# Kernel optimization log

Hardware: AMD Instinct MI355X
Metric: run time of the kernel (lower is better)

Reference implementation:

```python
import jax, jax.numpy as jnp
import numpy as np
import math

EMBED_DIM = 1024
NUM_HEADS = 16
B, T = 4, 2048
HEAD_DIM = EMBED_DIM // NUM_HEADS


def setup_inputs() -> dict:
    key = jax.random.key(0)
    ks = jax.random.split(key, 9)
    s = 1.0 / math.sqrt(EMBED_DIM)
    x = jax.random.normal(ks[0], (B, T, EMBED_DIM), dtype=jnp.float32)
    # causal mask, broadcastable over (B, H)
    mask = jnp.tril(jnp.ones((T, T), dtype=bool))[None, None, :, :]
    Wq = jax.random.normal(ks[1], (EMBED_DIM, EMBED_DIM), dtype=jnp.float32) * s
    bq = jnp.zeros((EMBED_DIM,), dtype=jnp.float32)
    Wk = jax.random.normal(ks[2], (EMBED_DIM, EMBED_DIM), dtype=jnp.float32) * s
    bk = jnp.zeros((EMBED_DIM,), dtype=jnp.float32)
    Wv = jax.random.normal(ks[3], (EMBED_DIM, EMBED_DIM), dtype=jnp.float32) * s
    bv = jnp.zeros((EMBED_DIM,), dtype=jnp.float32)
    Wo = jax.random.normal(ks[4], (EMBED_DIM, EMBED_DIM), dtype=jnp.float32) * s
    bo = jnp.zeros((EMBED_DIM,), dtype=jnp.float32)
    return {"x": x, "mask": mask, "Wq": Wq, "bq": bq, "Wk": Wk, "bk": bk,
            "Wv": Wv, "bv": bv, "Wo": Wo, "bo": bo}


def reference(x, mask, Wq, bq, Wk, bk, Wv, bv, Wo, bo):
    Bsz, Tlen, C = x.shape
    H, D = NUM_HEADS, HEAD_DIM
    q = (x @ Wq + bq).reshape(Bsz, Tlen, H, D).transpose(0, 2, 1, 3)  # [B,H,T,D]
    k = (x @ Wk + bk).reshape(Bsz, Tlen, H, D).transpose(0, 2, 1, 3)
    v = (x @ Wv + bv).reshape(Bsz, Tlen, H, D).transpose(0, 2, 1, 3)
    scores = jnp.einsum('bhtd,bhsd->bhts', q, k) / math.sqrt(D)  # [B,H,T,T]
    scores = jnp.where(mask, scores, jnp.float32(-1e9))
    attn = jax.nn.softmax(scores, axis=-1)
    out = jnp.einsum('bhts,bhsd->bhtd', attn, v)  # [B,H,T,D]
    out = out.transpose(0, 2, 1, 3).reshape(Bsz, Tlen, C)
    return out @ Wo + bo
```

## Files before the change

kernel.cpp:

```cpp
#include <hip/hip_runtime.h>

#define SEQ   2048
#define NH    16
#define HD    64
#define EMB   1024
#define NB    4
#define MTOT  (NB*SEQ)
#define NT    (SEQ/64)

typedef _Float16 f16;
typedef _Float16 f16x4 __attribute__((ext_vector_type(4)));
typedef _Float16 f16x8 __attribute__((ext_vector_type(8)));
typedef float    f32x4 __attribute__((ext_vector_type(4)));

#define MFMA_F16(a,b,c) __builtin_amdgcn_mfma_f32_16x16x32_f16(a,b,c,0,0,0)

#define QSCALE 0.18033688011112043f

__device__ __forceinline__ float fast_exp2(float x) {
#if __has_builtin(__builtin_amdgcn_exp2f)
  return __builtin_amdgcn_exp2f(x);
#else
  return exp2f(x);
#endif
}

__device__ __forceinline__ void gload16(const f16* g, f16* l) {
  __builtin_amdgcn_global_load_lds(
      (const __attribute__((address_space(1))) void*)g,
      (__attribute__((address_space(3))) void*)l, 16, 0, 0);
}

__global__ __launch_bounds__(256) void cast_x_kernel(
    const float* __restrict__ x, f16* __restrict__ xh) {
  size_t i = ((size_t)blockIdx.x * 256 + threadIdx.x) * 8;
  float4 a = *(const float4*)(x + i);
  float4 b = *(const float4*)(x + i + 4);
  f16x8 o;
  o[0]=(f16)a.x; o[1]=(f16)a.y; o[2]=(f16)a.z; o[3]=(f16)a.w;
  o[4]=(f16)b.x; o[5]=(f16)b.y; o[6]=(f16)b.z; o[7]=(f16)b.w;
  *(f16x8*)(xh + i) = o;
}

__global__ __launch_bounds__(256) void wtrans_kernel(
    const float* __restrict__ W0, const float* __restrict__ W1,
    const float* __restrict__ W2, const float* __restrict__ W3,
    f16* __restrict__ O0, f16* __restrict__ O1,
    f16* __restrict__ O2, f16* __restrict__ O3) {
  const int z = blockIdx.z;
  const float* W = (z==0)?W0:(z==1)?W1:(z==2)?W2:W3;
  f16* O        = (z==0)?O0:(z==1)?O1:(z==2)?O2:O3;
  __shared__ float Tl[64][68];
  const int t = threadIdx.x;
  const int k0 = blockIdx.x * 64, n0 = blockIdx.y * 64;
  {
    const int r = t >> 2, c0 = (t & 3) * 16;
    const float* src = W + (size_t)(k0 + r) * EMB + n0 + c0;
    #pragma unroll
    for (int j = 0; j < 4; ++j) {
      float4 v = *(const float4*)(src + 4 * j);
      Tl[c0+4*j+0][r]=v.x; Tl[c0+4*j+1][r]=v.y;
      Tl[c0+4*j+2][r]=v.z; Tl[c0+4*j+3][r]=v.w;
    }
  }
  __syncthreads();
  {
    const int n = t >> 2, c0 = (t & 3) * 16;
    f16* dst = O + (size_t)(n0 + n) * EMB + k0 + c0;
    #pragma unroll
    for (int j = 0; j < 2; ++j) {
      f16x8 o;
      #pragma unroll
      for (int u = 0; u < 8; ++u) o[u] = (f16)Tl[n][c0 + 8*j + u];
      *(f16x8*)(dst + 8 * j) = o;
    }
  }
}

template<int MODE>
__device__ __forceinline__ void gemm_core(
    const f16* __restrict__ A, const f16* __restrict__ Bt,
    const float* __restrict__ bias, void* __restrict__ out,
    int m0, int n0, float scale) {
  __shared__ f16 As[128 * 64];
  __shared__ f16 Bs[128 * 64];
  const int tid  = threadIdx.x;
  const int lane = tid & 63, w = tid >> 6;
  const int g = lane >> 4, lx = lane & 15;
  const int wr = w >> 1, wc = w & 1;
  const int sr = lane >> 3, sc = lane & 7;

  f32x4 acc[4][4];
  const f32x4 z4 = {0.f, 0.f, 0.f, 0.f};
  #pragma unroll
  for (int i = 0; i < 4; ++i)
    #pragma unroll
    for (int j = 0; j < 4; ++j) acc[i][j] = z4;

  for (int k0 = 0; k0 < EMB; k0 += 64) {
    __syncthreads();
    #pragma unroll
    for (int ci = 0; ci < 4; ++ci) {
      const int i = 4 * w + ci;
      const int r = i * 8 + sr;
      const int c = sc ^ (r & 7);
      gload16(A  + (size_t)(m0 + r) * EMB + k0 + c * 8, &As[i * 512]);
      gload16(Bt + (size_t)(n0 + r) * EMB + k0 + c * 8, &Bs[i * 512]);
    }
    __syncthreads();

    #pragma unroll
    for (int h = 0; h < 2; ++h) {
      f16x8 af[4], bf[4];
      #pragma unroll
      for (int mf = 0; mf < 4; ++mf) {
        const int row = wr * 64 + mf * 16 + lx;
        const int off = (row * 128 + h * 64 + g * 16) ^ ((row & 7) << 4);
        af[mf] = *(const f16x8*)((const char*)As + off);
      }
      #pragma unroll
      for (int nf = 0; nf < 4; ++nf) {
        const int row = wc * 64 + nf * 16 + lx;
        const int off = (row * 128 + h * 64 + g * 16) ^ ((row & 7) << 4);
        bf[nf] = *(const f16x8*)((const char*)Bs + off);
      }
      #pragma unroll
      for (int mf = 0; mf < 4; ++mf)
        #pragma unroll
        for (int nf = 0; nf < 4; ++nf)
          acc[mf][nf] = MFMA_F16(af[mf], bf[nf], acc[mf][nf]);
    }
  }

  #pragma unroll
  for (int mf = 0; mf < 4; ++mf) {
    #pragma unroll
    for (int nf = 0; nf < 4; ++nf) {
      const int n  = n0 + wc * 64 + nf * 16 + lx;
      const int mb = m0 + wr * 64 + mf * 16 + g * 4;
      const float bv = bias[n];
      if (MODE == 2) {
        float* op = (float*)out;
        #pragma unroll
        for (int r = 0; r < 4; ++r)
          op[(size_t)(mb + r) * EMB + n] = acc[mf][nf][r] + bv;
      } else {
        const int b = mb >> 11, tt = mb & (SEQ - 1);
        const int hh = n >> 6, d = n & (HD - 1);
        f16* op = (f16*)out;
        if (MODE == 0) {
          #pragma unroll
          for (int r = 0; r < 4; ++r)
            op[((size_t)(b * NH + hh) * SEQ + tt + r) * HD + d] =
                (f16)((acc[mf][nf][r] + bv) * scale);
        } else {
          f16x4 o;
          #pragma unroll
          for (int r = 0; r < 4; ++r) o[r] = (f16)(acc[mf][nf][r] + bv);
          *(f16x4*)(op + ((size_t)(b * NH + hh) * HD + d) * SEQ + tt) = o;
        }
      }
    }
  }
}

__global__ __launch_bounds__(256) void qkv_gemm_kernel(
    const f16* __restrict__ xh, const f16* __restrict__ wqt,
    const f16* __restrict__ wkt, const f16* __restrict__ wvt,
    const float* __restrict__ bq, const float* __restrict__ bk,
    const float* __restrict__ bv,
    f16* __restrict__ qh, f16* __restrict__ kh, f16* __restrict__ vth) {
  const int z = blockIdx.z;
  const int m0 = blockIdx.x * 128, n0 = blockIdx.y * 128;
  if (z == 0)      gemm_core<0>(xh, wqt, bq, qh, m0, n0, QSCALE);
  else if (z == 1) gemm_core<0>(xh, wkt, bk, kh, m0, n0, 1.0f);
  else             gemm_core<1>(xh, wvt, bv, vth, m0, n0, 1.0f);
}

__global__ __launch_bounds__(256) void proj_gemm_kernel(
    const f16* __restrict__ ath, const f16* __restrict__ wot,
    const float* __restrict__ bo, float* __restrict__ out) {
  gemm_core<2>(ath, wot, bo, out, blockIdx.x * 128, blockIdx.y * 128, 1.0f);
}

__global__ __launch_bounds__(256, 4) void attn_kernel(
    const f16* __restrict__ Qh, const f16* __restrict__ Kh,
    const f16* __restrict__ Vth, f16* __restrict__ Att) {
  __shared__ f16 Ks[64 * 64];
  __shared__ f16 Vs[64 * 64];
  __shared__ f16 Ps[4][16 * 64];
  const int tid  = threadIdx.x;
  const int lane = tid & 63, w = tid >> 6;
  const int g = lane >> 4, lx = lane & 15;
  const int sr = lane >> 3, sc = lane & 7;
  const int bid = blockIdx.x;
  const int xcd = bid & 7;
  const int idx = bid >> 3;
  const int p   = idx & 15;
  const int bh  = xcd + 8 * (idx >> 4);
  const int qlo = p, qhi = NT - 1 - p;
  const int nkt = qhi + 1;
  const f16* qp = Qh  + (size_t)bh * SEQ * HD;
  const f16* kp = Kh  + (size_t)bh * SEQ * HD;
  const f16* vp = Vth + (size_t)bh * HD * SEQ;
  const int row0[2] = {qlo * 64 + w * 16, qhi * 64 + w * 16};

  f16x8 qf[2][2];
  #pragma unroll
  for (int part = 0; part < 2; ++part) {
    const int qrow = row0[part] + lx;
    #pragma unroll
    for (int h = 0; h < 2; ++h)
      qf[part][h] = *(const f16x8*)(qp + (size_t)qrow * HD + h * 32 + g * 8);
  }

  const f32x4 z4 = {0.f, 0.f, 0.f, 0.f};
  f32x4 oa[2][4];
  float m_i[2] = {-1e30f, -1e30f}, l_i[2] = {0.f, 0.f};
  #pragma unroll
  for (int part = 0; part < 2; ++part)
    #pragma unroll
    for (int df = 0; df < 4; ++df) oa[part][df] = z4;

  for (int kt = 0; kt < nkt; ++kt) {
    __syncthreads();
    #pragma unroll
    for (int ci = 0; ci < 2; ++ci) {
      const int i = 2 * w + ci;
      const int r = i * 8 + sr;
      const int c = sc ^ (r & 7);
      gload16(kp + (size_t)(kt * 64 + r) * HD + c * 8, &Ks[i * 512]);
      gload16(vp + (size_t)r * SEQ + kt * 64 + c * 8,  &Vs[i * 512]);
    }
    __syncthreads();

    const int npart = (kt <= qlo) ? 2 : 1;
    #pragma unroll
    for (int pi = 0; pi < 2; ++pi) {
      if (pi >= npart) continue;
      const int part = 1 - pi;
      const int qrow = row0[part] + lx;
      const bool diag = (kt == (part ? qhi : qlo));

      f32x4 sa[4];
      #pragma unroll
      for (int sf = 0; sf < 4; ++sf) sa[sf] = z4;
      __builtin_amdgcn_s_setprio(1);
      #pragma unroll
      for (int h = 0; h < 2; ++h)
        #pragma unroll
        for (int sf = 0; sf < 4; ++sf) {
          const int row = sf * 16 + lx;
          const int off = (row * 128 + h * 64 + g * 16) ^ ((row & 7) << 4);
          f16x8 kf = *(const f16x8*)((const char*)Ks + off);
          sa[sf] = MFMA_F16(kf, qf[part][h], sa[sf]);
        }
      __builtin_amdgcn_s_setprio(0);

      float lmax = -1e30f;
      #pragma unroll
      for (int sf = 0; sf < 4; ++sf)
        #pragma unroll
        for (int r = 0; r < 4; ++r) {
          float vsc = sa[sf][r];
          if (diag) {
            const int kv = kt * 64 + sf * 16 + g * 4 + r;
            if (kv > qrow) { vsc = -1e30f; sa[sf][r] = vsc; }
          }
          lmax = fmaxf(lmax, vsc);
        }

      if (!__all(lmax <= m_i[part] + 8.f)) {
        float rmax = fmaxf(lmax, __shfl_xor(lmax, 16));
        rmax = fmaxf(rmax, __shfl_xor(rmax, 32));
        const float mnew = fmaxf(m_i[part], rmax);
        const float corr = fast_exp2(m_i[part] - mnew);
        m_i[part] = mnew;
        l_i[part] *= corr;
        #pragma unroll
        for (int r = 0; r < 4; ++r) {
          const float cr = __shfl(corr, g * 4 + r, 64);
          #pragma unroll
          for (int df = 0; df < 4; ++df) oa[part][df][r] *= cr;
        }
      }

      const float mcur = m_i[part];
      float rsum = 0.f;
      #pragma unroll
      for (int sf = 0; sf < 4; ++sf)
        #pragma unroll
        for (int r = 0; r < 4; ++r) {
          const float pv = fast_exp2(sa[sf][r] - mcur);
          sa[sf][r] = pv;
          rsum += pv;
        }
      l_i[part] += rsum;

      #pragma unroll
      for (int sf = 0; sf < 4; ++sf) {
        f16x4 p4;
        #pragma unroll
        for (int r = 0; r < 4; ++r) p4[r] = (f16)sa[sf][r];
        const int off = (lx * 128 + sf * 32 + g * 8) ^ ((lx & 7) << 4);
        *(f16x4*)((char*)Ps[w] + off) = p4;
      }

      __builtin_amdgcn_s_setprio(1);
      #pragma unroll
      for (int hk = 0; hk < 2; ++hk) {
        const int offp = (lx * 128 + hk * 64 + g * 16) ^ ((lx & 7) << 4);
        f16x8 pf = *(const f16x8*)((const char*)Ps[w] + offp);
        #pragma unroll
        for (int df = 0; df < 4; ++df) {
          const int row = df * 16 + lx;
          const int offv = (row * 128 + hk * 64 + g * 16) ^ ((row & 7) << 4);
          f16x8 vf = *(const f16x8*)((const char*)Vs + offv);
          oa[part][df] = MFMA_F16(pf, vf, oa[part][df]);
        }
      }
      __builtin_amdgcn_s_setprio(0);
    }
  }

  const int b = bh >> 4, hh = bh & 15;
  #pragma unroll
  for (int part = 0; part < 2; ++part) {
    float lf = l_i[part];
    lf += __shfl_xor(lf, 16);
    lf += __shfl_xor(lf, 32);
    const float inv = 1.f / lf;
    #pragma unroll
    for (int r = 0; r < 4; ++r) {
      const float ir = __shfl(inv, g * 4 + r, 64);
      const int t = row0[part] + g * 4 + r;
      f16* dst = Att + ((size_t)b * SEQ + t) * EMB + hh * HD;
      #pragma unroll
      for (int df = 0; df < 4; ++df)
        dst[df * 16 + lx] = (f16)(oa[part][df][r] * ir);
    }
  }
}

extern "C" void kernel_launch(void* const* d_in, const int* in_sizes, int n_in,
                              void* d_out, int out_size, void* d_ws, size_t ws_size,
                              hipStream_t stream) {
  (void)in_sizes; (void)n_in; (void)out_size; (void)ws_size;
  const float* x  = (const float*)d_in[0];
  const float* Wq = (const float*)d_in[2];
  const float* bq = (const float*)d_in[3];
  const float* Wk = (const float*)d_in[4];
  const float* bk = (const float*)d_in[5];
  const float* Wv = (const float*)d_in[6];
  const float* bv = (const float*)d_in[7];
  const float* Wo = (const float*)d_in[8];
  const float* bo = (const float*)d_in[9];

  f16* xh  = (f16*)d_ws;
  f16* wqt = xh  + (size_t)MTOT * EMB;
  f16* wkt = wqt + (size_t)EMB * EMB;
  f16* wvt = wkt + (size_t)EMB * EMB;
  f16* wot = wvt + (size_t)EMB * EMB;
  f16* qh  = wot + (size_t)EMB * EMB;
  f16* kh  = qh  + (size_t)MTOT * EMB;
  f16* vth = kh  + (size_t)MTOT * EMB;
  f16* ath = vth + (size_t)MTOT * EMB;

  cast_x_kernel<<<dim3(MTOT * EMB / (256 * 8)), 256, 0, stream>>>(x, xh);
  wtrans_kernel<<<dim3(16, 16, 4), 256, 0, stream>>>(
      Wq, Wk, Wv, Wo, wqt, wkt, wvt, wot);
  qkv_gemm_kernel<<<dim3(MTOT / 128, EMB / 128, 3), 256, 0, stream>>>(
      xh, wqt, wkt, wvt, bq, bk, bv, qh, kh, vth);
  attn_kernel<<<dim3((NT / 2) * NB * NH), 256, 0, stream>>>(qh, kh, vth, ath);
  proj_gemm_kernel<<<dim3(MTOT / 128, EMB / 128), 256, 0, stream>>>(
      ath, wot, bo, (float*)d_out);
}
```

Baseline: 223.9 us.

## Split attention KV loop across two blocks and merge partials in a combine kernel

```diff
diff --git a/kernel.cpp b/kernel.cpp
--- a/kernel.cpp
+++ b/kernel.cpp
@@ -185,7 +185,8 @@
 
 __global__ __launch_bounds__(256, 4) void attn_kernel(
     const f16* __restrict__ Qh, const f16* __restrict__ Kh,
-    const f16* __restrict__ Vth, f16* __restrict__ Att) {
+    const f16* __restrict__ Vth, f16* __restrict__ Opart,
+    float* __restrict__ mPart, float* __restrict__ lPart) {
   __shared__ f16 Ks[64 * 64];
   __shared__ f16 Vs[64 * 64];
   __shared__ f16 Ps[4][16 * 64];
@@ -194,10 +195,11 @@
   const int g = lane >> 4, lx = lane & 15;
   const int sr = lane >> 3, sc = lane & 7;
   const int bid = blockIdx.x;
-  const int xcd = bid & 7;
-  const int idx = bid >> 3;
-  const int p   = idx & 15;
-  const int bh  = xcd + 8 * (idx >> 4);
+  const int xcd   = bid & 7;
+  const int idx   = bid >> 3;
+  const int split = idx & 1;
+  const int p     = (idx >> 1) & 15;
+  const int bh    = xcd + 8 * (idx >> 5);
   const int qlo = p, qhi = NT - 1 - p;
   const int nkt = qhi + 1;
   const f16* qp = Qh  + (size_t)bh * SEQ * HD;
@@ -222,7 +224,7 @@
     #pragma unroll
     for (int df = 0; df < 4; ++df) oa[part][df] = z4;
 
-  for (int kt = 0; kt < nkt; ++kt) {
+  for (int kt = split; kt < nkt; kt += 2) {
     __syncthreads();
     #pragma unroll
     for (int ci = 0; ci < 2; ++ci) {
@@ -257,7 +259,7 @@
         }
       __builtin_amdgcn_s_setprio(0);
 
-      float lmax = -1e30f;
+      float rmax = -1e30f;
       #pragma unroll
       for (int sf = 0; sf < 4; ++sf)
         #pragma unroll
@@ -265,37 +267,28 @@
           float vsc = sa[sf][r];
           if (diag) {
             const int kv = kt * 64 + sf * 16 + g * 4 + r;
-            if (kv > qrow) { vsc = -1e30f; sa[sf][r] = vsc; }
+            if (kv > qrow) vsc = -1e30f;
           }
-          lmax = fmaxf(lmax, vsc);
+          sa[sf][r] = vsc;
+          rmax = fmaxf(rmax, vsc);
         }
-
-      if (!__all(lmax <= m_i[part] + 8.f)) {
-        float rmax = fmaxf(lmax, __shfl_xor(lmax, 16));
-        rmax = fmaxf(rmax, __shfl_xor(rmax, 32));
-        const float mnew = fmaxf(m_i[part], rmax);
-        const float corr = fast_exp2(m_i[part] - mnew);
-        m_i[part] = mnew;
-        l_i[part] *= corr;
+      rmax = fmaxf(rmax, __shfl_xor(rmax, 16));
+      rmax = fmaxf(rmax, __shfl_xor(rmax, 32));
+      const float mnew = fmaxf(m_i[part], rmax);
+      const float corr = fast_exp2(m_i[part] - mnew);
+      m_i[part] = mnew;
+      float rsum = 0.f;
+      #pragma unroll
+      for (int sf = 0; sf < 4; ++sf)
         #pragma unroll
         for (int r = 0; r < 4; ++r) {
-          const float cr = __shfl(corr, g * 4 + r, 64);
-          #pragma unroll
-          for (int df = 0; df < 4; ++df) oa[part][df][r] *= cr;
-        }
-      }
-
-      const float mcur = m_i[part];
-      float rsum = 0.f;
-      #pragma unroll
-      for (int sf = 0; sf < 4; ++sf)
-        #pragma unroll
-        for (int r = 0; r < 4; ++r) {
-          const float pv = fast_exp2(sa[sf][r] - mcur);
+          const float pv = fast_exp2(sa[sf][r] - mnew);
           sa[sf][r] = pv;
           rsum += pv;
         }
-      l_i[part] += rsum;
+      rsum += __shfl_xor(rsum, 16);
+      rsum += __shfl_xor(rsum, 32);
+      l_i[part] = l_i[part] * corr + rsum;
 
       #pragma unroll
       for (int sf = 0; sf < 4; ++sf) {
@@ -304,6 +297,13 @@
         for (int r = 0; r < 4; ++r) p4[r] = (f16)sa[sf][r];
         const int off = (lx * 128 + sf * 32 + g * 8) ^ ((lx & 7) << 4);
         *(f16x4*)((char*)Ps[w] + off) = p4;
+      }
+
+      #pragma unroll
+      for (int r = 0; r < 4; ++r) {
+        const float cr = __shfl(corr, g * 4 + r, 64);
+        #pragma unroll
+        for (int df = 0; df < 4; ++df) oa[part][df][r] *= cr;
       }
 
       __builtin_amdgcn_s_setprio(1);
@@ -323,23 +323,46 @@
     }
   }
 
-  const int b = bh >> 4, hh = bh & 15;
+  const size_t sb = (size_t)split * 64 + bh;
   #pragma unroll
   for (int part = 0; part < 2; ++part) {
-    float lf = l_i[part];
-    lf += __shfl_xor(lf, 16);
-    lf += __shfl_xor(lf, 32);
-    const float inv = 1.f / lf;
+    if (lane < 16) {
+      mPart[sb * SEQ + row0[part] + lane] = m_i[part];
+      lPart[sb * SEQ + row0[part] + lane] = l_i[part];
+    }
     #pragma unroll
     for (int r = 0; r < 4; ++r) {
-      const float ir = __shfl(inv, g * 4 + r, 64);
       const int t = row0[part] + g * 4 + r;
-      f16* dst = Att + ((size_t)b * SEQ + t) * EMB + hh * HD;
+      f16* dst = Opart + ((size_t)sb * SEQ + t) * HD;
       #pragma unroll
       for (int df = 0; df < 4; ++df)
-        dst[df * 16 + lx] = (f16)(oa[part][df][r] * ir);
-    }
-  }
+        dst[df * 16 + lx] = (f16)(oa[part][df][r]);
+    }
+  }
+}
+
+__global__ __launch_bounds__(256) void combine_kernel(
+    const f16* __restrict__ Opart, const float* __restrict__ mPart,
+    const float* __restrict__ lPart, f16* __restrict__ Att) {
+  const int G = blockIdx.x * 256 + threadIdx.x;
+  const int chunk = G & 7;
+  const int rowid = G >> 3;
+  const int bh = rowid >> 11, t = rowid & (SEQ - 1);
+  const int b = bh >> 4, h = bh & 15;
+  const size_t i1 = (size_t)bh * SEQ + t;
+  const size_t i2 = (size_t)(64 + bh) * SEQ + t;
+  const float m1 = mPart[i1], m2 = mPart[i2];
+  const float l1 = lPart[i1], l2 = lPart[i2];
+  const float mx = fmaxf(m1, m2);
+  const float w1 = fast_exp2(m1 - mx), w2 = fast_exp2(m2 - mx);
+  const float inv = 1.f / (l1 * w1 + l2 * w2);
+  const f16x8 o1 = *(const f16x8*)(Opart + i1 * HD + chunk * 8);
+  const f16x8 o2 = *(const f16x8*)(Opart + i2 * HD + chunk * 8);
+  f16x8 o;
+  #pragma unroll
+  for (int j = 0; j < 8; ++j)
+    o[j] = (f16)(((float)o1[j] * w1 + (float)o2[j] * w2) * inv);
+  *(f16x8*)(Att + ((size_t)b * SEQ + t) * EMB + h * HD + chunk * 8) = o;
 }
 
 extern "C" void kernel_launch(void* const* d_in, const int* in_sizes, int n_in,
@@ -356,22 +379,28 @@
   const float* Wo = (const float*)d_in[8];
   const float* bo = (const float*)d_in[9];
 
-  f16* xh  = (f16*)d_ws;
-  f16* wqt = xh  + (size_t)MTOT * EMB;
-  f16* wkt = wqt + (size_t)EMB * EMB;
-  f16* wvt = wkt + (size_t)EMB * EMB;
-  f16* wot = wvt + (size_t)EMB * EMB;
-  f16* qh  = wot + (size_t)EMB * EMB;
-  f16* kh  = qh  + (size_t)MTOT * EMB;
-  f16* vth = kh  + (size_t)MTOT * EMB;
-  f16* ath = vth + (size_t)MTOT * EMB;
+  f16* xh    = (f16*)d_ws;
+  f16* wqt   = xh  + (size_t)MTOT * EMB;
+  f16* wkt   = wqt + (size_t)EMB * EMB;
+  f16* wvt   = wkt + (size_t)EMB * EMB;
+  f16* wot   = wvt + (size_t)EMB * EMB;
+  f16* qh    = wot + (size_t)EMB * EMB;
+  f16* kh    = qh  + (size_t)MTOT * EMB;
+  f16* vth   = kh  + (size_t)MTOT * EMB;
+  f16* ath   = vth + (size_t)MTOT * EMB;
+  f16* Opart = ath + (size_t)MTOT * EMB;
+  float* mP  = (float*)(Opart + (size_t)2 * 64 * SEQ * HD);
+  float* lP  = mP + (size_t)2 * 64 * SEQ;
 
   cast_x_kernel<<<dim3(MTOT * EMB / (256 * 8)), 256, 0, stream>>>(x, xh);
   wtrans_kernel<<<dim3(16, 16, 4), 256, 0, stream>>>(
       Wq, Wk, Wv, Wo, wqt, wkt, wvt, wot);
   qkv_gemm_kernel<<<dim3(MTOT / 128, EMB / 128, 3), 256, 0, stream>>>(
       xh, wqt, wkt, wvt, bq, bk, bv, qh, kh, vth);
-  attn_kernel<<<dim3((NT / 2) * NB * NH), 256, 0, stream>>>(qh, kh, vth, ath);
+  attn_kernel<<<dim3((NT / 2) * 2 * NB * NH), 256, 0, stream>>>(
+      qh, kh, vth, Opart, mP, lP);
+  combine_kernel<<<dim3(NB * NH * SEQ * 8 / 256), 256, 0, stream>>>(
+      Opart, mP, lP, ath);
   proj_gemm_kernel<<<dim3(MTOT / 128, EMB / 128), 256, 0, stream>>>(
       ath, wot, bo, (float*)d_out);
 }
```

After: 192.5 us. -14.0%, faster.
